# Performance work log

Hardware: AMD Instinct MI355X
Metric: run time of the kernel (lower is better)

## Reference

```python
import jax, jax.numpy as jnp
import numpy as np

N = 100000          # nodes
E = 1600000         # edges
NODE_DIM = 128
EDGE_DIM = 1
EMB = 16            # out_channels per head
H = 2               # heads
HID = 32
OUT = 2
NEG_SLOPE = 0.2


def gatv2_layer(x, src, dst, eattr, Wl, bl, Wr, br, We, att, bias):
    """PyG GATv2Conv: add self-loops (edge_attr fill='mean'), edge attention,
    segment softmax over target nodes, scatter-add aggregation, concat heads."""
    n = x.shape[0]
    heads, ch = att.shape
    # --- add self loops; self-loop edge_attr = mean of incoming edge_attr per node ---
    ones = jnp.ones((src.shape[0],), dtype=x.dtype)
    deg = jax.ops.segment_sum(ones, dst, num_segments=n)
    loop_attr = jax.ops.segment_sum(eattr, dst, num_segments=n) / jnp.maximum(deg, 1.0)[:, None]
    idx = jnp.arange(n, dtype=src.dtype)
    src2 = jnp.concatenate([src, idx])
    dst2 = jnp.concatenate([dst, idx])
    eattr2 = jnp.concatenate([eattr, loop_attr], axis=0)
    # --- linear projections ---
    xl = (x @ Wl + bl).reshape(n, heads, ch)   # source-side (lin_l)
    xr = (x @ Wr + br).reshape(n, heads, ch)   # target-side (lin_r)
    ef = (eattr2 @ We).reshape(-1, heads, ch)  # edge features (lin_edge, no bias)
    # --- per-edge attention logits (GATv2: LeakyReLU inside, then att dot) ---
    e = xl[src2] + xr[dst2] + ef               # [E2, H, C]
    e = jnp.where(e >= 0, e, NEG_SLOPE * e)
    logits = jnp.einsum('ehc,hc->eh', e, att)  # [E2, H]
    # --- segment softmax over edges sharing the same target node ---
    m = jax.ops.segment_max(logits, dst2, num_segments=n)      # [N, H]
    a = jnp.exp(logits - m[dst2])
    denom = jax.ops.segment_sum(a, dst2, num_segments=n)
    alpha = a / denom[dst2]                                    # [E2, H]
    # --- scatter-add weighted source messages ---
    msg = (alpha[:, :, None] * xl[src2]).reshape(-1, heads * ch)
    out = jax.ops.segment_sum(msg, dst2, num_segments=n)       # [N, H*C]
    return out + bias


def setup_inputs() -> dict:
    key = jax.random.key(0)
    ks = jax.random.split(key, 24)
    p = lambda k, s: (jax.random.normal(k, s, dtype=jnp.float32) * 0.1)
    HC = H * EMB
    return {
        'x': jax.random.normal(ks[0], (N, NODE_DIM), dtype=jnp.float32),
        'edge_index': jax.random.randint(ks[1], (2, E), 0, N, dtype=jnp.int32),
        'edge_attr': jax.random.normal(ks[2], (E, EDGE_DIM), dtype=jnp.float32),
        # layer 1
        'Wl1': p(ks[3], (NODE_DIM, HC)), 'bl1': p(ks[4], (HC,)),
        'Wr1': p(ks[5], (NODE_DIM, HC)), 'br1': p(ks[6], (HC,)),
        'We1': p(ks[7], (EDGE_DIM, HC)), 'att1': p(ks[8], (H, EMB)), 'b1': p(ks[9], (HC,)),
        # layer 2 (input dim = H*EMB)
        'Wl2': p(ks[10], (HC, HC)), 'bl2': p(ks[11], (HC,)),
        'Wr2': p(ks[12], (HC, HC)), 'br2': p(ks[13], (HC,)),
        'We2': p(ks[14], (EDGE_DIM, HC)), 'att2': p(ks[15], (H, EMB)), 'b2': p(ks[16], (HC,)),
        # decoder MLP
        'Wd1': p(ks[17], (HC, HID)), 'bd1': p(ks[18], (HID,)),
        'Wd2': p(ks[19], (HID, OUT)), 'bd2': p(ks[20], (OUT,)),
    }


def reference(x, edge_index, edge_attr,
              Wl1, bl1, Wr1, br1, We1, att1, b1,
              Wl2, bl2, Wr2, br2, We2, att2, b2,
              Wd1, bd1, Wd2, bd2):
    src, dst = edge_index[0], edge_index[1]
    h = gatv2_layer(x, src, dst, edge_attr, Wl1, bl1, Wr1, br1, We1, att1, b1)
    h = gatv2_layer(h, src, dst, edge_attr, Wl2, bl2, Wr2, br2, We2, att2, b2)
    h = jax.nn.relu(h @ Wd1 + bd1)
    return h @ Wd2 + bd2
```

## Files before the change

kernel.cpp:

```cpp
#include <hip/hip_runtime.h>
#include <hip/hip_fp16.h>
#include <math.h>


#define NN 100000
#define NE 1600000
#define SLOT 48
#define CSTRIDE 16
#define NEG_SLOPE 0.2f

__global__ void scatter_kernel(const int* __restrict__ src, const int* __restrict__ dst,
                               const float* __restrict__ eattr,
                               int* __restrict__ counts, unsigned* __restrict__ pay) {
    int e = blockIdx.x * blockDim.x + threadIdx.x;
    if (e >= NE) return;
    int d = dst[e];
    int pos = atomicAdd(counts + (size_t)d * CSTRIDE, 1);
    if (pos < SLOT) {
        unsigned hb = __half_as_ushort(__float2half_rn(eattr[e]));
        pay[(size_t)d * SLOT + pos] = ((unsigned)src[e] << 15) | (hb >> 1);
    }
}

__device__ __forceinline__ float pk_ea(unsigned p) {
    return __half2float(__ushort_as_half((unsigned short)((p & 0x7FFFu) << 1)));
}
__device__ __forceinline__ float lrelu(float v) {
    return (v >= 0.f) ? v : NEG_SLOPE * v;
}

template <int K>
__global__ void proj_kernel(const float* __restrict__ x,
                            const float* __restrict__ Wl, const float* __restrict__ bl,
                            const float* __restrict__ Wr, const float* __restrict__ br,
                            __half* __restrict__ xl, float* __restrict__ xr) {
    __shared__ __align__(16) float sWl[K * 32];
    __shared__ __align__(16) float sWr[K * 32];
    __shared__ float sb[64];
    for (int i = threadIdx.x; i < K * 32; i += blockDim.x) {
        int k = i >> 5, col = i & 31;
        int p = (((k >> 2) ^ (col & 7)) << 2) | (k & 3);
        sWl[col * K + p] = Wl[i];
        sWr[col * K + p] = Wr[i];
    }
    if (threadIdx.x < 32) sb[threadIdx.x] = bl[threadIdx.x];
    else if (threadIdx.x < 64) sb[threadIdx.x] = br[threadIdx.x - 32];
    __syncthreads();
    int t = blockIdx.x * blockDim.x + threadIdx.x;
    int g = t >> 5, col = t & 31;
    int row0 = g * 4;
    if (row0 >= NN) return;
    const float4* x0 = (const float4*)(x + (size_t)(row0 + 0) * K);
    const float4* x1 = (const float4*)(x + (size_t)(row0 + 1) * K);
    const float4* x2 = (const float4*)(x + (size_t)(row0 + 2) * K);
    const float4* x3 = (const float4*)(x + (size_t)(row0 + 3) * K);
    const float4* wl4 = (const float4*)(sWl + col * K);
    const float4* wr4 = (const float4*)(sWr + col * K);
    int swz = col & 7;
    float al0 = 0.f, al1 = 0.f, al2 = 0.f, al3 = 0.f;
    float ar0 = 0.f, ar1 = 0.f, ar2 = 0.f, ar3 = 0.f;
#pragma unroll 4
    for (int k4 = 0; k4 < K / 4; k4++) {
        float4 wl = wl4[k4 ^ swz];
        float4 wr = wr4[k4 ^ swz];
        float4 a = x0[k4];
        float4 b = x1[k4];
        float4 c = x2[k4];
        float4 d = x3[k4];
        al0 = fmaf(a.x, wl.x, al0); al0 = fmaf(a.y, wl.y, al0);
        al0 = fmaf(a.z, wl.z, al0); al0 = fmaf(a.w, wl.w, al0);
        ar0 = fmaf(a.x, wr.x, ar0); ar0 = fmaf(a.y, wr.y, ar0);
        ar0 = fmaf(a.z, wr.z, ar0); ar0 = fmaf(a.w, wr.w, ar0);
        al1 = fmaf(b.x, wl.x, al1); al1 = fmaf(b.y, wl.y, al1);
        al1 = fmaf(b.z, wl.z, al1); al1 = fmaf(b.w, wl.w, al1);
        ar1 = fmaf(b.x, wr.x, ar1); ar1 = fmaf(b.y, wr.y, ar1);
        ar1 = fmaf(b.z, wr.z, ar1); ar1 = fmaf(b.w, wr.w, ar1);
        al2 = fmaf(c.x, wl.x, al2); al2 = fmaf(c.y, wl.y, al2);
        al2 = fmaf(c.z, wl.z, al2); al2 = fmaf(c.w, wl.w, al2);
        ar2 = fmaf(c.x, wr.x, ar2); ar2 = fmaf(c.y, wr.y, ar2);
        ar2 = fmaf(c.z, wr.z, ar2); ar2 = fmaf(c.w, wr.w, ar2);
        al3 = fmaf(d.x, wl.x, al3); al3 = fmaf(d.y, wl.y, al3);
        al3 = fmaf(d.z, wl.z, al3); al3 = fmaf(d.w, wl.w, al3);
        ar3 = fmaf(d.x, wr.x, ar3); ar3 = fmaf(d.y, wr.y, ar3);
        ar3 = fmaf(d.z, wr.z, ar3); ar3 = fmaf(d.w, wr.w, ar3);
    }
    float bls = sb[col], brs = sb[32 + col];
    xl[(size_t)(row0 + 0) * 32 + col] = __float2half_rn(al0 + bls);
    xr[(size_t)(row0 + 0) * 32 + col] = ar0 + brs;
    xl[(size_t)(row0 + 1) * 32 + col] = __float2half_rn(al1 + bls);
    xr[(size_t)(row0 + 1) * 32 + col] = ar1 + brs;
    xl[(size_t)(row0 + 2) * 32 + col] = __float2half_rn(al2 + bls);
    xr[(size_t)(row0 + 2) * 32 + col] = ar2 + brs;
    xl[(size_t)(row0 + 3) * 32 + col] = __float2half_rn(al3 + bls);
    xr[(size_t)(row0 + 3) * 32 + col] = ar3 + brs;
}

__device__ __forceinline__ void gat_core4(const int* __restrict__ counts,
                                          const unsigned* __restrict__ pay,
                                          const __half* xl, const float* xr,
                                          const float* We, const float* att,
                                          const float* bias, int node, int L,
                                          float h[4]) {
    int k = L & 7, j = L >> 3;
    int cnt = counts[(size_t)node * CSTRIDE];
    int deg = (cnt < SLOT) ? cnt : SLOT;
    const unsigned* row = pay + (size_t)node * SLOT;
    float4 we = ((const float4*)We)[k];
    float4 at = ((const float4*)att)[k];
    float4 xrc = ((const float4*)(xr + (size_t)node * 32))[k];
    ushort4 sq = ((const ushort4*)(xl + (size_t)node * 32))[k];
    float sx0 = __half2float(__ushort_as_half(sq.x));
    float sx1 = __half2float(__ushort_as_half(sq.y));
    float sx2 = __half2float(__ushort_as_half(sq.z));
    float sx3 = __half2float(__ushort_as_half(sq.w));
    float ssum = 0.f, a0 = 0.f, a1 = 0.f, a2 = 0.f, a3 = 0.f, easum = 0.f;
    unsigned pv_c = row[j];
    int n1 = j + 4; if (n1 > SLOT - 1) n1 = SLOT - 1;
    unsigned pv_n = row[n1];
    bool val_c = j < deg;
    int s_c = val_c ? (int)(pv_c >> 15) : 0;
    ushort4 q_c = ((const ushort4*)(xl + (size_t)s_c * 32))[k];
    for (int base = 0; base < deg; base += 4) {
        int idx = base + j;
        bool val_n = (idx + 4) < deg;
        int s_n = val_n ? (int)(pv_n >> 15) : 0;
        ushort4 q_n = ((const ushort4*)(xl + (size_t)s_n * 32))[k];
        int n2 = idx + 8; if (n2 > SLOT - 1) n2 = SLOT - 1;
        unsigned pv_n2 = row[n2];
        float ea = pk_ea(pv_c);
        float x0 = __half2float(__ushort_as_half(q_c.x));
        float x1 = __half2float(__ushort_as_half(q_c.y));
        float x2 = __half2float(__ushort_as_half(q_c.z));
        float x3 = __half2float(__ushort_as_half(q_c.w));
        float p;
        p  = at.x * lrelu(fmaf(ea, we.x, x0 + xrc.x));
        p  = fmaf(at.y, lrelu(fmaf(ea, we.y, x1 + xrc.y)), p);
        p  = fmaf(at.z, lrelu(fmaf(ea, we.z, x2 + xrc.z)), p);
        p  = fmaf(at.w, lrelu(fmaf(ea, we.w, x3 + xrc.w)), p);
        p += __shfl_xor(p, 1);
        p += __shfl_xor(p, 2);
        float w = val_c ? __expf(p) : 0.f;
        ssum += w;
        easum += val_c ? ea : 0.f;
        a0 = fmaf(w, x0, a0);
        a1 = fmaf(w, x1, a1);
        a2 = fmaf(w, x2, a2);
        a3 = fmaf(w, x3, a3);
        pv_c = pv_n; pv_n = pv_n2; q_c = q_n; val_c = val_n;
    }
    ssum  += __shfl_xor(ssum, 8);   ssum  += __shfl_xor(ssum, 16);
    easum += __shfl_xor(easum, 8);  easum += __shfl_xor(easum, 16);
    a0 += __shfl_xor(a0, 8);  a0 += __shfl_xor(a0, 16);
    a1 += __shfl_xor(a1, 8);  a1 += __shfl_xor(a1, 16);
    a2 += __shfl_xor(a2, 8);  a2 += __shfl_xor(a2, 16);
    a3 += __shfl_xor(a3, 8);  a3 += __shfl_xor(a3, 16);
    {
        float ea0 = easum / fmaxf((float)cnt, 1.f);
        float p;
        p  = at.x * lrelu(fmaf(ea0, we.x, sx0 + xrc.x));
        p  = fmaf(at.y, lrelu(fmaf(ea0, we.y, sx1 + xrc.y)), p);
        p  = fmaf(at.z, lrelu(fmaf(ea0, we.z, sx2 + xrc.z)), p);
        p  = fmaf(at.w, lrelu(fmaf(ea0, we.w, sx3 + xrc.w)), p);
        p += __shfl_xor(p, 1);
        p += __shfl_xor(p, 2);
        float w = __expf(p);
        ssum += w;
        a0 = fmaf(w, sx0, a0);
        a1 = fmaf(w, sx1, a1);
        a2 = fmaf(w, sx2, a2);
        a3 = fmaf(w, sx3, a3);
    }
    float4 bq = ((const float4*)bias)[k];
    float inv = 1.f / ssum;
    h[0] = a0 * inv + bq.x;
    h[1] = a1 * inv + bq.y;
    h[2] = a2 * inv + bq.z;
    h[3] = a3 * inv + bq.w;
}

#define HBUF_FENCE() do { \
    asm volatile("s_waitcnt lgkmcnt(0)" ::: "memory"); \
    __builtin_amdgcn_sched_barrier(0); \
} while (0)

__global__ void gat1_proj2_kernel(const int* __restrict__ counts,
                                  const unsigned* __restrict__ pay,
                                  const __half* __restrict__ xl, const float* __restrict__ xr,
                                  const float* __restrict__ We, const float* __restrict__ att,
                                  const float* __restrict__ bias,
                                  const float* __restrict__ Wl2, const float* __restrict__ bl2,
                                  const float* __restrict__ Wr2, const float* __restrict__ br2,
                                  __half* __restrict__ xl2, float* __restrict__ xr2) {
    __shared__ __align__(16) float sWl[1024];
    __shared__ __align__(16) float sWr[1024];
    __shared__ float4 hbuf[8][8];
    for (int i = threadIdx.x; i < 1024; i += blockDim.x) {
        int cc = i >> 5, Lc = i & 31;
        int p = (((cc >> 2) ^ (Lc & 7)) << 2) | (cc & 3);
        sWl[Lc * 32 + p] = Wl2[i];
        sWr[Lc * 32 + p] = Wr2[i];
    }
    __syncthreads();
    int t = blockIdx.x * blockDim.x + threadIdx.x;
    int node = t >> 5, L = t & 31;
    if (node >= NN) return;
    float h[4];
    gat_core4(counts, pay, xl, xr, We, att, bias, node, L, h);
    int nl = threadIdx.x >> 5;
    if (L < 8) hbuf[nl][L] = make_float4(h[0], h[1], h[2], h[3]);
    HBUF_FENCE();
    const float4* hv4 = hbuf[nl];
    const float4* wl4 = (const float4*)(sWl + L * 32);
    const float4* wr4 = (const float4*)(sWr + L * 32);
    int swz = L & 7;
    float al = bl2[L], ar = br2[L];
#pragma unroll
    for (int c4 = 0; c4 < 8; c4++) {
        float4 hv = hv4[c4];
        float4 wl = wl4[c4 ^ swz];
        float4 wr = wr4[c4 ^ swz];
        al = fmaf(hv.x, wl.x, al); al = fmaf(hv.y, wl.y, al);
        al = fmaf(hv.z, wl.z, al); al = fmaf(hv.w, wl.w, al);
        ar = fmaf(hv.x, wr.x, ar); ar = fmaf(hv.y, wr.y, ar);
        ar = fmaf(hv.z, wr.z, ar); ar = fmaf(hv.w, wr.w, ar);
    }
    xl2[(size_t)node * 32 + L] = __float2half_rn(al);
    xr2[(size_t)node * 32 + L] = ar;
}

__global__ void gat2_dec_kernel(const int* __restrict__ counts,
                                const unsigned* __restrict__ pay,
                                const __half* __restrict__ xl, const float* __restrict__ xr,
                                const float* __restrict__ We, const float* __restrict__ att,
                                const float* __restrict__ bias,
                                const float* __restrict__ Wd1, const float* __restrict__ bd1,
                                const float* __restrict__ Wd2, const float* __restrict__ bd2,
                                float* __restrict__ out) {
    __shared__ __align__(16) float sWd1[1024];
    __shared__ float sWd2[64];
    __shared__ float4 hbuf[8][8];
    for (int i = threadIdx.x; i < 1024; i += blockDim.x) {
        int cc = i >> 5, Lc = i & 31;
        int p = (((cc >> 2) ^ (Lc & 7)) << 2) | (cc & 3);
        sWd1[Lc * 32 + p] = Wd1[i];
    }
    if (threadIdx.x < 64) sWd2[threadIdx.x] = Wd2[threadIdx.x];
    __syncthreads();
    int t = blockIdx.x * blockDim.x + threadIdx.x;
    int node = t >> 5, L = t & 31;
    if (node >= NN) return;
    float h[4];
    gat_core4(counts, pay, xl, xr, We, att, bias, node, L, h);
    int nl = threadIdx.x >> 5;
    if (L < 8) hbuf[nl][L] = make_float4(h[0], h[1], h[2], h[3]);
    HBUF_FENCE();
    const float4* hv4 = hbuf[nl];
    const float4* wd4 = (const float4*)(sWd1 + L * 32);
    int swz = L & 7;
    float d1 = bd1[L];
#pragma unroll
    for (int c4 = 0; c4 < 8; c4++) {
        float4 hv = hv4[c4];
        float4 wd = wd4[c4 ^ swz];
        d1 = fmaf(hv.x, wd.x, d1); d1 = fmaf(hv.y, wd.y, d1);
        d1 = fmaf(hv.z, wd.z, d1); d1 = fmaf(hv.w, wd.w, d1);
    }
    float hid = fmaxf(d1, 0.f);
    float o0 = hid * sWd2[L * 2 + 0];
    float o1 = hid * sWd2[L * 2 + 1];
    o0 += __shfl_xor(o0, 1);   o1 += __shfl_xor(o1, 1);
    o0 += __shfl_xor(o0, 2);   o1 += __shfl_xor(o1, 2);
    o0 += __shfl_xor(o0, 4);   o1 += __shfl_xor(o1, 4);
    o0 += __shfl_xor(o0, 8);   o1 += __shfl_xor(o1, 8);
    o0 += __shfl_xor(o0, 16);  o1 += __shfl_xor(o1, 16);
    if (L == 0) {
        out[(size_t)node * 2 + 0] = o0 + bd2[0];
        out[(size_t)node * 2 + 1] = o1 + bd2[1];
    }
}

extern "C" void kernel_launch(void* const* d_in, const int* in_sizes, int n_in,
                              void* d_out, int out_size, void* d_ws, size_t ws_size,
                              hipStream_t stream) {
    const float* x     = (const float*)d_in[0];
    const int*   src   = (const int*)d_in[1];
    const int*   dst   = src + NE;
    const float* eattr = (const float*)d_in[2];
    const float* Wl1 = (const float*)d_in[3],  *bl1 = (const float*)d_in[4];
    const float* Wr1 = (const float*)d_in[5],  *br1 = (const float*)d_in[6];
    const float* We1 = (const float*)d_in[7],  *att1 = (const float*)d_in[8];
    const float* b1  = (const float*)d_in[9];
    const float* Wl2 = (const float*)d_in[10], *bl2 = (const float*)d_in[11];
    const float* Wr2 = (const float*)d_in[12], *br2 = (const float*)d_in[13];
    const float* We2 = (const float*)d_in[14], *att2 = (const float*)d_in[15];
    const float* b2  = (const float*)d_in[16];
    const float* Wd1 = (const float*)d_in[17], *bd1 = (const float*)d_in[18];
    const float* Wd2 = (const float*)d_in[19], *bd2 = (const float*)d_in[20];
    float* out = (float*)d_out;

    char* w = (char*)d_ws;
    int*      counts = (int*)w;       w += (size_t)NN * CSTRIDE * 4;
    unsigned* pay    = (unsigned*)w;  w += (size_t)NN * SLOT * 4;
    __half*   xl  = (__half*)w;       w += (size_t)NN * 32 * 2;
    float*    xr  = (float*)w;        w += (size_t)NN * 32 * 4;
    __half*   xl2 = (__half*)w;       w += (size_t)NN * 32 * 2;
    float*    xr2 = (float*)w;        w += (size_t)NN * 32 * 4;

    const int B = 256;
    const int gE   = NE / B;
    const int gN32 = (NN * 32) / B;
    const int gP   = (NN / 4 * 32) / B;

    hipMemsetAsync(counts, 0, (size_t)NN * CSTRIDE * 4, stream);
    scatter_kernel<<<gE, B, 0, stream>>>(src, dst, eattr, counts, pay);

    proj_kernel<128><<<gP, B, 0, stream>>>(x, Wl1, bl1, Wr1, br1, xl, xr);

    gat1_proj2_kernel<<<gN32, B, 0, stream>>>(counts, pay, xl, xr, We1, att1, b1,
                                              Wl2, bl2, Wr2, br2, xl2, xr2);

    gat2_dec_kernel<<<gN32, B, 0, stream>>>(counts, pay, xl2, xr2, We2, att2, b2,
                                            Wd1, bd1, Wd2, bd2, out);
}
```

Before: 409.4 us.

## Merge edge counts into per-node CSR rows and partition scatter by destination

The separate padded count array and payload array become one 256-byte row per node, with the counter in the first word and payload slots starting at offset 4. Counter and payload now share cache lines for both the scatter atomics and the GAT gathers. The scatter kernel is launched with 8x more blocks, and each block handles only destinations whose low 3 bits match its partition. This is meant to localize atomic traffic, but every block re-reads the dst array, so dst reads rise eightfold and most threads exit early. The memset also grows because each row is 256 bytes.

```diff
diff --git a/kernel.cpp b/kernel.cpp
--- a/kernel.cpp
+++ b/kernel.cpp
@@ -6,19 +6,23 @@
 #define NN 100000
 #define NE 1600000
 #define SLOT 48
-#define CSTRIDE 16
+#define ROWU 64
+#define NPART 8
 #define NEG_SLOPE 0.2f
 
 __global__ void scatter_kernel(const int* __restrict__ src, const int* __restrict__ dst,
                                const float* __restrict__ eattr,
-                               int* __restrict__ counts, unsigned* __restrict__ pay) {
-    int e = blockIdx.x * blockDim.x + threadIdx.x;
-    if (e >= NE) return;
+                               unsigned* __restrict__ csr) {
+    int part = blockIdx.x & (NPART - 1);
+    int chunk = blockIdx.x >> 3;
+    int e = chunk * blockDim.x + threadIdx.x;
     int d = dst[e];
-    int pos = atomicAdd(counts + (size_t)d * CSTRIDE, 1);
+    if ((d & (NPART - 1)) != part) return;
+    unsigned* row = csr + (size_t)d * ROWU;
+    int pos = atomicAdd((int*)row, 1);
     if (pos < SLOT) {
         unsigned hb = __half_as_ushort(__float2half_rn(eattr[e]));
-        pay[(size_t)d * SLOT + pos] = ((unsigned)src[e] << 15) | (hb >> 1);
+        row[4 + pos] = ((unsigned)src[e] << 15) | (hb >> 1);
     }
 }
 
@@ -82,7 +86,7 @@
         al3 = fmaf(d.x, wl.x, al3); al3 = fmaf(d.y, wl.y, al3);
         al3 = fmaf(d.z, wl.z, al3); al3 = fmaf(d.w, wl.w, al3);
         ar3 = fmaf(d.x, wr.x, ar3); ar3 = fmaf(d.y, wr.y, ar3);
-        ar3 = fmaf(d.z, wr.z, ar3); ar3 = fmaf(d.w, wr.w, ar3);
+        ar3 = fmaf(d.w, wr.w, ar3); ar3 = fmaf(d.z, wr.z, ar3);
     }
     float bls = sb[col], brs = sb[32 + col];
     xl[(size_t)(row0 + 0) * 32 + col] = __float2half_rn(al0 + bls);
@@ -95,16 +99,15 @@
     xr[(size_t)(row0 + 3) * 32 + col] = ar3 + brs;
 }
 
-__device__ __forceinline__ void gat_core4(const int* __restrict__ counts,
-                                          const unsigned* __restrict__ pay,
+__device__ __forceinline__ void gat_core4(const unsigned* __restrict__ csr,
                                           const __half* xl, const float* xr,
                                           const float* We, const float* att,
                                           const float* bias, int node, int L,
                                           float h[4]) {
     int k = L & 7, j = L >> 3;
-    int cnt = counts[(size_t)node * CSTRIDE];
+    const unsigned* row = csr + (size_t)node * ROWU;
+    int cnt = (int)row[0];
     int deg = (cnt < SLOT) ? cnt : SLOT;
-    const unsigned* row = pay + (size_t)node * SLOT;
     float4 we = ((const float4*)We)[k];
     float4 at = ((const float4*)att)[k];
     float4 xrc = ((const float4*)(xr + (size_t)node * 32))[k];
@@ -114,9 +117,9 @@
     float sx2 = __half2float(__ushort_as_half(sq.z));
     float sx3 = __half2float(__ushort_as_half(sq.w));
     float ssum = 0.f, a0 = 0.f, a1 = 0.f, a2 = 0.f, a3 = 0.f, easum = 0.f;
-    unsigned pv_c = row[j];
+    unsigned pv_c = row[4 + j];
     int n1 = j + 4; if (n1 > SLOT - 1) n1 = SLOT - 1;
-    unsigned pv_n = row[n1];
+    unsigned pv_n = row[4 + n1];
     bool val_c = j < deg;
     int s_c = val_c ? (int)(pv_c >> 15) : 0;
     ushort4 q_c = ((const ushort4*)(xl + (size_t)s_c * 32))[k];
@@ -126,7 +129,7 @@
         int s_n = val_n ? (int)(pv_n >> 15) : 0;
         ushort4 q_n = ((const ushort4*)(xl + (size_t)s_n * 32))[k];
         int n2 = idx + 8; if (n2 > SLOT - 1) n2 = SLOT - 1;
-        unsigned pv_n2 = row[n2];
+        unsigned pv_n2 = row[4 + n2];
         float ea = pk_ea(pv_c);
         float x0 = __half2float(__ushort_as_half(q_c.x));
         float x1 = __half2float(__ushort_as_half(q_c.y));
@@ -183,8 +186,7 @@
     __builtin_amdgcn_sched_barrier(0); \
 } while (0)
 
-__global__ void gat1_proj2_kernel(const int* __restrict__ counts,
-                                  const unsigned* __restrict__ pay,
+__global__ void gat1_proj2_kernel(const unsigned* __restrict__ csr,
                                   const __half* __restrict__ xl, const float* __restrict__ xr,
                                   const float* __restrict__ We, const float* __restrict__ att,
                                   const float* __restrict__ bias,
@@ -205,7 +207,7 @@
     int node = t >> 5, L = t & 31;
     if (node >= NN) return;
     float h[4];
-    gat_core4(counts, pay, xl, xr, We, att, bias, node, L, h);
+    gat_core4(csr, xl, xr, We, att, bias, node, L, h);
     int nl = threadIdx.x >> 5;
     if (L < 8) hbuf[nl][L] = make_float4(h[0], h[1], h[2], h[3]);
     HBUF_FENCE();
@@ -228,8 +230,7 @@
     xr2[(size_t)node * 32 + L] = ar;
 }
 
-__global__ void gat2_dec_kernel(const int* __restrict__ counts,
-                                const unsigned* __restrict__ pay,
+__global__ void gat2_dec_kernel(const unsigned* __restrict__ csr,
                                 const __half* __restrict__ xl, const float* __restrict__ xr,
                                 const float* __restrict__ We, const float* __restrict__ att,
                                 const float* __restrict__ bias,
@@ -250,7 +251,7 @@
     int node = t >> 5, L = t & 31;
     if (node >= NN) return;
     float h[4];
-    gat_core4(counts, pay, xl, xr, We, att, bias, node, L, h);
+    gat_core4(csr, xl, xr, We, att, bias, node, L, h);
     int nl = threadIdx.x >> 5;
     if (L < 8) hbuf[nl][L] = make_float4(h[0], h[1], h[2], h[3]);
     HBUF_FENCE();
@@ -299,26 +300,25 @@
     float* out = (float*)d_out;
 
     char* w = (char*)d_ws;
-    int*      counts = (int*)w;       w += (size_t)NN * CSTRIDE * 4;
-    unsigned* pay    = (unsigned*)w;  w += (size_t)NN * SLOT * 4;
-    __half*   xl  = (__half*)w;       w += (size_t)NN * 32 * 2;
-    float*    xr  = (float*)w;        w += (size_t)NN * 32 * 4;
-    __half*   xl2 = (__half*)w;       w += (size_t)NN * 32 * 2;
-    float*    xr2 = (float*)w;        w += (size_t)NN * 32 * 4;
+    unsigned* csr = (unsigned*)w;  w += (size_t)NN * ROWU * 4;
+    __half*   xl  = (__half*)w;    w += (size_t)NN * 32 * 2;
+    float*    xr  = (float*)w;     w += (size_t)NN * 32 * 4;
+    __half*   xl2 = (__half*)w;    w += (size_t)NN * 32 * 2;
+    float*    xr2 = (float*)w;     w += (size_t)NN * 32 * 4;
 
     const int B = 256;
-    const int gE   = NE / B;
+    const int gE   = (NE / B) * NPART;
     const int gN32 = (NN * 32) / B;
     const int gP   = (NN / 4 * 32) / B;
 
-    hipMemsetAsync(counts, 0, (size_t)NN * CSTRIDE * 4, stream);
-    scatter_kernel<<<gE, B, 0, stream>>>(src, dst, eattr, counts, pay);
+    hipMemsetAsync(csr, 0, (size_t)NN * ROWU * 4, stream);
+    scatter_kernel<<<gE, B, 0, stream>>>(src, dst, eattr, csr);
 
     proj_kernel<128><<<gP, B, 0, stream>>>(x, Wl1, bl1, Wr1, br1, xl, xr);
 
-    gat1_proj2_kernel<<<gN32, B, 0, stream>>>(counts, pay, xl, xr, We1, att1, b1,
+    gat1_proj2_kernel<<<gN32, B, 0, stream>>>(csr, xl, xr, We1, att1, b1,
                                               Wl2, bl2, Wr2, br2, xl2, xr2);
 
-    gat2_dec_kernel<<<gN32, B, 0, stream>>>(counts, pay, xl2, xr2, We2, att2, b2,
+    gat2_dec_kernel<<<gN32, B, 0, stream>>>(csr, xl2, xr2, We2, att2, b2,
                                             Wd1, bd1, Wd2, bd2, out);
 }
```

Measured after the change: 441.4 us. 7.8% more time.
